# Kernel optimization log

Measured on AMD Instinct MI355X. Metric: run time of the kernel, lower is better.

## Reference

```python
import jax, jax.numpy as jnp
import numpy as np

IMG = 256
CUT_RATE = 0.1
CUT_LEN = int(IMG * CUT_RATE)      # 25
REMAIN = (IMG - CUT_LEN) // 2      # 115
CROP = 2 * REMAIN                  # 230  (crop window is always CROP x CROP)


def _cut_start(index):
    # vectorized cut_location(); window length is always CROP, return left edge a
    xy = IMG - index
    return jnp.where(index <= REMAIN, 0,
           jnp.where(xy <= REMAIN, IMG - CROP, index - REMAIN)).astype(jnp.int32)


def _bilinear_crop(img, x0, y0):
    # img: [C, IMG, IMG]; crop CROP x CROP window at (x0, y0) and resize to
    # IMG x IMG with bilinear, align_corners=True (matches F.interpolate).
    scale = (CROP - 1) / (IMG - 1)
    src = jnp.arange(IMG, dtype=img.dtype) * scale        # [IMG] source coords in crop
    i0 = jnp.floor(src).astype(jnp.int32)
    i1 = jnp.minimum(i0 + 1, CROP - 1)
    w = src - i0.astype(img.dtype)                        # [IMG] frac weights
    r0, r1 = x0 + i0, x0 + i1                             # absolute row indices
    c0, c1 = y0 + i0, y0 + i1                             # absolute col indices
    top = img[:, r0, :]                                   # [C, IMG, IMG]
    bot = img[:, r1, :]
    rows = top * (1.0 - w)[None, :, None] + bot * w[None, :, None]
    left = rows[:, :, c0]
    right = rows[:, :, c1]
    return left * (1.0 - w)[None, None, :] + right * w[None, None, :]


def setup_inputs() -> dict:
    key = jax.random.key(0)
    k1, k2 = jax.random.split(key)
    x = jax.random.normal(k1, (128, 3, 256, 256), dtype=jnp.float32)
    feature_map = jax.random.normal(k2, (128, 512, 16, 16), dtype=jnp.float32)
    return {"x": x, "feature_map": feature_map}


def reference(x, feature_map):
    B, C, H, W = feature_map.shape
    # SE-style weighting: global avg pool per channel, relu(weight * fm)
    fw = feature_map.mean(axis=(2, 3), keepdims=True)     # [B,C,1,1]
    se = jax.nn.relu(fw * feature_map)                    # [B,C,H,W]
    cam = se.mean(axis=1)                                 # [B,H,W] channel-mean CAM
    idx = jnp.argmax(cam.reshape(B, -1), axis=1)          # flat argmax per sample
    fx = idx // H                                         # torch uses feature_size[0]
    fy = idx % W
    ix = (IMG * fx) // H                                  # map to image coords
    iy = (IMG * fy) // W
    x_left = _cut_start(ix)
    y_top = _cut_start(iy)
    out = jax.vmap(_bilinear_crop)(x, x_left, y_top)      # [B,3,256,256]
    # torch clones+detaches the crop; output carries no gradient
    return jax.lax.stop_gradient(out)
```

## Files before the change

### kernel.cpp

```cpp
#include <hip/hip_runtime.h>

#define IMG 256
#define CROPW 230
#define REMAIN 115
#define NGROUP 16
#define GCH    32
#define TILE_I 16
#define MAXROWS 16
#define NTILE  16
#define TPB    3

__device__ __forceinline__ int cut_start(int v) {
    int xy = IMG - v;
    return (v <= REMAIN) ? 0 : ((xy <= REMAIN) ? (IMG - CROPW) : (v - REMAIN));
}

__device__ __forceinline__ void load_row16(const float* g, float* l) {
    __builtin_amdgcn_global_load_lds(
        (const __attribute__((address_space(1))) void*)g,
        (__attribute__((address_space(3))) void*)l,
        16, 0, 0);
}

__global__ __launch_bounds__(256) void cam_partial_kernel(
    const float* __restrict__ fm, float* __restrict__ cam_part)
{
    const int blk = blockIdx.x;
    const int b = blk >> 4;
    const int g = blk & (NGROUP - 1);
    const int tid = threadIdx.x;
    const int lane = tid & 63;
    const int wave = tid >> 6;

    __shared__ float tile[GCH * 256];
    __shared__ float fw[GCH];

    const float* src = fm + ((size_t)b * 512 + (size_t)g * GCH) * 256;

    const float4* src4 = (const float4*)src;
    float4* tile4 = (float4*)tile;
    #pragma unroll
    for (int k = 0; k < 8; ++k)
        tile4[tid + k * 256] = src4[tid + k * 256];
    __syncthreads();

    for (int c = wave * 8; c < wave * 8 + 8; ++c) {
        const float* row = tile + c * 256;
        float s = row[lane] + row[lane + 64] + row[lane + 128] + row[lane + 192];
        #pragma unroll
        for (int off = 32; off >= 1; off >>= 1)
            s += __shfl_xor(s, off, 64);
        if (lane == 0) fw[c] = s * (1.0f / 256.0f);
    }
    __syncthreads();

    float acc = 0.0f;
    #pragma unroll
    for (int c = 0; c < GCH; ++c) {
        float v = fw[c] * tile[c * 256 + tid];
        acc += (v > 0.0f) ? v : 0.0f;
    }
    cam_part[(size_t)blk * 256 + tid] = acc;
}

__global__ __launch_bounds__(256) void argmax_kernel(
    const float* __restrict__ cam_part, int* __restrict__ se_out)
{
    const int b = blockIdx.x;
    const int tid = threadIdx.x;

    __shared__ float s_val[256];
    __shared__ int   s_idx[256];

    float acc = 0.0f;
    #pragma unroll
    for (int g = 0; g < NGROUP; ++g)
        acc += cam_part[((size_t)b * NGROUP + g) * 256 + tid];

    s_val[tid] = acc;
    s_idx[tid] = tid;
    __syncthreads();

    for (int stride = 128; stride >= 1; stride >>= 1) {
        if (tid < stride) {
            float v2 = s_val[tid + stride]; int i2 = s_idx[tid + stride];
            float v1 = s_val[tid];          int i1 = s_idx[tid];
            if (v2 > v1 || (v2 == v1 && i2 < i1)) { s_val[tid] = v2; s_idx[tid] = i2; }
        }
        __syncthreads();
    }

    if (tid == 0) {
        int idx = s_idx[0];
        int fx = idx >> 4, fy = idx & 15;
        int ix = 16 * fx,  iy = 16 * fy;
        se_out[2 * b]     = cut_start(ix);
        se_out[2 * b + 1] = cut_start(iy);
    }
}

__global__ __launch_bounds__(256) void bilinear_dma_kernel(
    const float* __restrict__ x, const int* __restrict__ se, float* __restrict__ out)
{
    __shared__ float buf[2][MAXROWS * 256];

    const int tid  = threadIdx.x;
    const int wave = tid >> 6;
    const int lane = tid & 63;
    const float scale = (float)(229.0 / 255.0);

    const int t0 = blockIdx.x * TPB;
    const int jp  = tid & 127;
    const int ilh = tid >> 7;

    {
        const int bc = t0 >> 4;
        const int ib = (t0 & (NTILE - 1)) * TILE_I;
        const int b  = bc / 3;
        const int x0 = se[2 * b];
        const int r_first = x0 + (int)floorf((float)ib * scale);
        const float* img = x + (size_t)bc * (IMG * IMG);
        #pragma unroll
        for (int k = 0; k < 4; ++k) {
            const int r = wave * 4 + k;
            const int srow = min(r_first + r, IMG - 1);
            load_row16(img + srow * IMG + lane * 4, &buf[0][r * 256]);
        }
    }
    asm volatile("s_waitcnt vmcnt(0)" ::: "memory");
    __syncthreads();

    for (int it = 0; it < TPB; ++it) {
        const int t   = t0 + it;
        const int cur = it & 1;
        const int bc  = t >> 4;
        const int ib  = (t & (NTILE - 1)) * TILE_I;
        const int b   = bc / 3;
        const int x0  = se[2 * b];
        const int y0  = se[2 * b + 1];
        const int r_first = x0 + (int)floorf((float)ib * scale);

        if (it + 1 < TPB) {
            const int tn  = t + 1;
            const int bcn = tn >> 4;
            const int ibn = (tn & (NTILE - 1)) * TILE_I;
            const int bn  = bcn / 3;
            const int x0n = se[2 * bn];
            const int rfn = x0n + (int)floorf((float)ibn * scale);
            const float* imgn = x + (size_t)bcn * (IMG * IMG);
            #pragma unroll
            for (int k = 0; k < 4; ++k) {
                const int r = wave * 4 + k;
                const int srow = min(rfn + r, IMG - 1);
                load_row16(imgn + srow * IMG + lane * 4, &buf[cur ^ 1][r * 256]);
            }
        }

        const float* rows = buf[cur];

        const int   ja  = 2 * jp;
        const float sja = (float)ja * scale;
        const int   j0a = (int)floorf(sja);
        const float wja = sja - (float)j0a;
        const int   c0a = y0 + j0a;

        const int   jb  = ja + 1;
        const float sjb = (float)jb * scale;
        const int   j0b = (int)floorf(sjb);
        const float wjb = sjb - (float)j0b;
        const int   c1b = y0 + min(j0b + 1, CROPW - 1);
        const bool  bstep = (j0b != j0a);

        float2* outp2 = (float2*)(out + (size_t)bc * (IMG * IMG) + (size_t)ib * IMG) + jp;

        #pragma unroll
        for (int iter = 0; iter < TILE_I / 2; ++iter) {
            const int   il = 2 * iter + ilh;
            const int   i  = ib + il;
            const float si = (float)i * scale;
            const int   i0 = (int)floorf(si);
            const float wi = si - (float)i0;
            const int   i1 = min(i0 + 1, CROPW - 1);
            const int   row0 = (x0 + i0 - r_first) << 8;
            const int   row1 = (x0 + i1 - r_first) << 8;
            const float owi = 1.0f - wi;

            const float t0v = rows[row0 + c0a];
            const float t1v = rows[row0 + c0a + 1];
            const float txv = rows[row0 + c1b];
            const float u0v = rows[row1 + c0a];
            const float u1v = rows[row1 + c0a + 1];
            const float uxv = rows[row1 + c1b];

            const float la = t0v * owi + u0v * wi;
            const float ra = t1v * owi + u1v * wi;
            const float oa = la * (1.0f - wja) + ra * wja;

            const float tb = bstep ? t1v : t0v;
            const float ub = bstep ? u1v : u0v;
            const float lb = tb * owi + ub * wi;
            const float rb = txv * owi + uxv * wi;
            const float ob = lb * (1.0f - wjb) + rb * wjb;

            outp2[il * 128] = make_float2(oa, ob);
        }

        asm volatile("s_waitcnt vmcnt(0)" ::: "memory");
        __syncthreads();
    }
}

extern "C" void kernel_launch(void* const* d_in, const int* in_sizes, int n_in,
                              void* d_out, int out_size, void* d_ws, size_t ws_size,
                              hipStream_t stream) {
    const float* x  = (const float*)d_in[0];
    const float* fm = (const float*)d_in[1];
    float* out = (float*)d_out;

    int*   se       = (int*)d_ws;
    float* cam_part = (float*)((char*)d_ws + 1024);

    cam_partial_kernel<<<128 * NGROUP, 256, 0, stream>>>(fm, cam_part);
    argmax_kernel<<<128, 256, 0, stream>>>(cam_part, se);

    bilinear_dma_kernel<<<2048, 256, 0, stream>>>(x, se, out);
}
```

Before: 53.52 us.

## Replace LDS-DMA double buffer with register prefetch and nontemporal stores

The bilinear kernel no longer uses global_load_lds into a double-buffered LDS array. It prefetches the next tile's 16 source rows into float4 registers while computing the current tile, then writes them into a single LDS buffer between two barriers. Output stores become nontemporal vector stores so the large write stream does not pollute the cache. This halves LDS use per block, which may raise occupancy. In exchange it costs extra VGPRs and an added barrier per tile.

```diff
diff --git a/kernel.cpp b/kernel.cpp
--- a/kernel.cpp
+++ b/kernel.cpp
@@ -10,16 +10,11 @@
 #define NTILE  16
 #define TPB    3
 
+typedef float f32x2 __attribute__((ext_vector_type(2)));
+
 __device__ __forceinline__ int cut_start(int v) {
     int xy = IMG - v;
     return (v <= REMAIN) ? 0 : ((xy <= REMAIN) ? (IMG - CROPW) : (v - REMAIN));
-}
-
-__device__ __forceinline__ void load_row16(const float* g, float* l) {
-    __builtin_amdgcn_global_load_lds(
-        (const __attribute__((address_space(1))) void*)g,
-        (__attribute__((address_space(3))) void*)l,
-        16, 0, 0);
 }
 
 __global__ __launch_bounds__(256) void cam_partial_kernel(
@@ -99,45 +94,47 @@
     }
 }
 
-__global__ __launch_bounds__(256) void bilinear_dma_kernel(
+__global__ __launch_bounds__(256) void bilinear_pipe_kernel(
     const float* __restrict__ x, const int* __restrict__ se, float* __restrict__ out)
 {
-    __shared__ float buf[2][MAXROWS * 256];
+    __shared__ float rows[MAXROWS * 256];
+    float4* rows4 = (float4*)rows;
 
     const int tid  = threadIdx.x;
     const int wave = tid >> 6;
     const int lane = tid & 63;
+    const int jp   = tid & 127;
+    const int ilh  = tid >> 7;
     const float scale = (float)(229.0 / 255.0);
 
     const int t0 = blockIdx.x * TPB;
-    const int jp  = tid & 127;
-    const int ilh = tid >> 7;
-
+
+    float4 n0, n1, n2, n3;
     {
         const int bc = t0 >> 4;
         const int ib = (t0 & (NTILE - 1)) * TILE_I;
         const int b  = bc / 3;
         const int x0 = se[2 * b];
-        const int r_first = x0 + (int)floorf((float)ib * scale);
-        const float* img = x + (size_t)bc * (IMG * IMG);
-        #pragma unroll
-        for (int k = 0; k < 4; ++k) {
-            const int r = wave * 4 + k;
-            const int srow = min(r_first + r, IMG - 1);
-            load_row16(img + srow * IMG + lane * 4, &buf[0][r * 256]);
-        }
-    }
-    asm volatile("s_waitcnt vmcnt(0)" ::: "memory");
+        const int rf = x0 + (int)floorf((float)ib * scale);
+        const float4* img4 = (const float4*)(x + (size_t)bc * (IMG * IMG));
+        n0 = img4[min(rf + 4 * 0 + wave, IMG - 1) * 64 + lane];
+        n1 = img4[min(rf + 4 * 1 + wave, IMG - 1) * 64 + lane];
+        n2 = img4[min(rf + 4 * 2 + wave, IMG - 1) * 64 + lane];
+        n3 = img4[min(rf + 4 * 3 + wave, IMG - 1) * 64 + lane];
+    }
+    rows4[tid + 0 * 256] = n0;
+    rows4[tid + 1 * 256] = n1;
+    rows4[tid + 2 * 256] = n2;
+    rows4[tid + 3 * 256] = n3;
     __syncthreads();
 
     for (int it = 0; it < TPB; ++it) {
-        const int t   = t0 + it;
-        const int cur = it & 1;
-        const int bc  = t >> 4;
-        const int ib  = (t & (NTILE - 1)) * TILE_I;
-        const int b   = bc / 3;
-        const int x0  = se[2 * b];
-        const int y0  = se[2 * b + 1];
+        const int t  = t0 + it;
+        const int bc = t >> 4;
+        const int ib = (t & (NTILE - 1)) * TILE_I;
+        const int b  = bc / 3;
+        const int x0 = se[2 * b];
+        const int y0 = se[2 * b + 1];
         const int r_first = x0 + (int)floorf((float)ib * scale);
 
         if (it + 1 < TPB) {
@@ -147,16 +144,12 @@
             const int bn  = bcn / 3;
             const int x0n = se[2 * bn];
             const int rfn = x0n + (int)floorf((float)ibn * scale);
-            const float* imgn = x + (size_t)bcn * (IMG * IMG);
-            #pragma unroll
-            for (int k = 0; k < 4; ++k) {
-                const int r = wave * 4 + k;
-                const int srow = min(rfn + r, IMG - 1);
-                load_row16(imgn + srow * IMG + lane * 4, &buf[cur ^ 1][r * 256]);
-            }
-        }
-
-        const float* rows = buf[cur];
+            const float4* img4 = (const float4*)(x + (size_t)bcn * (IMG * IMG));
+            n0 = img4[min(rfn + 4 * 0 + wave, IMG - 1) * 64 + lane];
+            n1 = img4[min(rfn + 4 * 1 + wave, IMG - 1) * 64 + lane];
+            n2 = img4[min(rfn + 4 * 2 + wave, IMG - 1) * 64 + lane];
+            n3 = img4[min(rfn + 4 * 3 + wave, IMG - 1) * 64 + lane];
+        }
 
         const int   ja  = 2 * jp;
         const float sja = (float)ja * scale;
@@ -171,7 +164,7 @@
         const int   c1b = y0 + min(j0b + 1, CROPW - 1);
         const bool  bstep = (j0b != j0a);
 
-        float2* outp2 = (float2*)(out + (size_t)bc * (IMG * IMG) + (size_t)ib * IMG) + jp;
+        f32x2* outp2 = (f32x2*)(out + (size_t)bc * (IMG * IMG) + (size_t)ib * IMG) + jp;
 
         #pragma unroll
         for (int iter = 0; iter < TILE_I / 2; ++iter) {
@@ -202,11 +195,18 @@
             const float rb = txv * owi + uxv * wi;
             const float ob = lb * (1.0f - wjb) + rb * wjb;
 
-            outp2[il * 128] = make_float2(oa, ob);
-        }
-
-        asm volatile("s_waitcnt vmcnt(0)" ::: "memory");
-        __syncthreads();
+            f32x2 o2; o2.x = oa; o2.y = ob;
+            __builtin_nontemporal_store(o2, &outp2[il * 128]);
+        }
+
+        if (it + 1 < TPB) {
+            __syncthreads();
+            rows4[tid + 0 * 256] = n0;
+            rows4[tid + 1 * 256] = n1;
+            rows4[tid + 2 * 256] = n2;
+            rows4[tid + 3 * 256] = n3;
+            __syncthreads();
+        }
     }
 }
 
@@ -223,5 +223,5 @@
     cam_partial_kernel<<<128 * NGROUP, 256, 0, stream>>>(fm, cam_part);
     argmax_kernel<<<128, 256, 0, stream>>>(cam_part, se);
 
-    bilinear_dma_kernel<<<2048, 256, 0, stream>>>(x, se, out);
-}
+    bilinear_pipe_kernel<<<2048, 256, 0, stream>>>(x, se, out);
+}
```

Result: faster. 52.08 us (-2.7%).
